# Optimization experiments

Hardware: AMD Instinct MI355X
Metric: run time of the kernel (lower is better)

## Reference

```python
import jax, jax.numpy as jnp
import numpy as np

N_E, E_DIM = 1024, 256

def setup_inputs() -> dict:
    key = jax.random.key(0)
    k1, k2 = jax.random.split(key)
    z = jax.random.normal(k1, (16, E_DIM, 64, 64), dtype=jnp.float32)
    codebook = jax.random.normal(k2, (N_E, E_DIM), dtype=jnp.float32)
    return {"z": z, "codebook": codebook}

def reference(z, codebook):
    B, C, H, W = z.shape  # C == e_dim
    zp = jnp.transpose(z, (0, 2, 3, 1))          # B,H,W,C
    zf = zp.reshape(-1, C)                        # N,C with N=B*H*W
    # L2 distance: ||z||^2 + ||c||^2 - 2 z c^T  -> [N, n_e]
    d = (jnp.sum(zf * zf, axis=1, keepdims=True)
         + jnp.sum(codebook * codebook, axis=1)
         - 2.0 * jnp.matmul(zf, codebook.T))
    idx = jnp.argmin(d, axis=1)                   # [N] int
    # one-hot @ codebook == gather (same math)
    z_q = codebook[idx].reshape(zp.shape)         # B,H,W,C
    codebook_loss = jnp.mean((z_q - jax.lax.stop_gradient(zp)) ** 2)
    z_q_out = jnp.transpose(z_q, (0, 3, 1, 2))    # B,C,H,W
    min_encoding_indices = idx.reshape(B, 1, H, W)
    return (z_q_out, codebook_loss, jnp.zeros((), z_q_out.dtype), min_encoding_indices)
```

## Files before the change

kernel.cpp:

```cpp
#include <hip/hip_runtime.h>

#define HW 4096
#define NE 1024
#define LOSS_OFF 16777216
#define IDX_OFF  16777218
#define MARGIN 0.08f

typedef __attribute__((ext_vector_type(8))) _Float16 half8v;
typedef __attribute__((ext_vector_type(4))) float float4v;

#define WS_LIST_OFF   64
#define WS_CNORM_OFF  262208
#define WS_CBH_OFF    266304
#define WS_PART_OFF   790592

__device__ __forceinline__ unsigned short f16rne(float f) {
    _Float16 h = (_Float16)f;
    return __builtin_bit_cast(unsigned short, h);
}

__device__ __forceinline__ unsigned f16pk(float a, float b) {
    auto h = __builtin_amdgcn_cvt_pkrtz(a, b);
    return __builtin_bit_cast(unsigned, h);
}

__device__ __forceinline__ void stage16(const void* g, void* l) {
    __builtin_amdgcn_global_load_lds(
        (const __attribute__((address_space(1))) unsigned*)g,
        (__attribute__((address_space(3))) unsigned*)l, 16, 0, 0);
}

__global__ __launch_bounds__(256) void k0_prep(const float* __restrict__ cb,
                                               float* __restrict__ cnorm,
                                               unsigned short* __restrict__ cbh,
                                               int* __restrict__ flagcnt) {
    const int tid = threadIdx.x;
    if (blockIdx.x == 0 && tid == 0) *flagcnt = 0;
    const int e = blockIdx.x * 64 + (tid >> 2);
    const int j = tid & 3;
    const float4* src = (const float4*)(cb + (size_t)e * 256 + j * 64);
    unsigned short* dst = cbh + (size_t)e * 256 + j * 64;
    float s = 0.f;
#pragma unroll
    for (int i = 0; i < 16; ++i) {
        float4 v = src[i];
        s += v.x * v.x + v.y * v.y + v.z * v.z + v.w * v.w;
        unsigned p0 = (unsigned)f16rne(v.x) | ((unsigned)f16rne(v.y) << 16);
        unsigned p1 = (unsigned)f16rne(v.z) | ((unsigned)f16rne(v.w) << 16);
        *(uint2*)(dst + i * 4) = make_uint2(p0, p1);
    }
    s += __shfl_xor(s, 1, 64);
    s += __shfl_xor(s, 2, 64);
    if (j == 0) cnorm[e] = 0.5f * s;
}

__global__ __launch_bounds__(256, 3) void k1_mfma(const float* __restrict__ z,
                                                  const unsigned short* __restrict__ cbh,
                                                  const float* __restrict__ cnorm,
                                                  float* __restrict__ out_idx,
                                                  int* __restrict__ flagcnt,
                                                  int* __restrict__ flaglist) {
    __shared__ __align__(16) char smem[34304];
    char* bufs = smem;
    float* cand1 = (float*)(smem + 32768);
    int*   candi = (int*)  (smem + 33280);
    float* cand2 = (float*)(smem + 33792);

    const int tid = threadIdx.x;
    const int lane = tid & 63, w = tid >> 6;
    const int wx = w & 1, wy = w >> 1;
    const int lr = lane & 15, lg = lane >> 4;
    const unsigned bswz = (unsigned)(lr << 4);

    const int n0 = blockIdx.x * 64;
    const int hw0 = n0 & 4095;
    const float* zb = z + (size_t)(n0 >> 12) * (256 * HW);
    const char* cbh_b = (const char*)cbh;

    {
        const int row = tid & 63, kg8 = tid >> 6;
        const unsigned zswz = (unsigned)((row & 15) << 4);
#pragma unroll
        for (int it = 0; it < 8; ++it) {
            int kb = (kg8 + it * 4) * 8;
            float v[8];
#pragma unroll
            for (int q = 0; q < 8; ++q) v[q] = zb[(size_t)(kb + q) * HW + hw0 + row];
            unsigned pk[4];
#pragma unroll
            for (int q = 0; q < 4; ++q) pk[q] = f16pk(v[2*q], v[2*q+1]);
            unsigned scol = (unsigned)(kb * 2) ^ zswz;
            *(int4*)(smem + row * 512 + scol) = make_int4(pk[0], pk[1], pk[2], pk[3]);
        }
    }
    __syncthreads();

    half8v A[2][8];
#pragma unroll
    for (int mi = 0; mi < 2; ++mi)
#pragma unroll
        for (int ks = 0; ks < 8; ++ks)
            A[mi][ks] = *(const half8v*)(smem + (32*wy + 16*mi + lr) * 512
                                              + ((unsigned)(64*ks + 16*lg) ^ bswz));
    __syncthreads();

    const int i0 = w * 4;
    const int elo_half = lane >> 5;
    const unsigned col0 = (unsigned)((lane & 31) * 16);

#pragma unroll
    for (int i = 0; i < 4; ++i) {
        int e_loc = 2 * (i0 + i) + elo_half;
        unsigned col = col0 ^ (unsigned)((e_loc & 15) << 4);
        stage16(cbh_b + (size_t)e_loc * 512 + col, bufs + (i0 + i) * 1024);
    }
    __syncthreads();

    const float* cnp = cnorm + 16 * wx + lr;
    float b1[8], b2[8]; int bi[8];
#pragma unroll
    for (int i = 0; i < 8; ++i) { b1[i] = 1e30f; b2[i] = 1e30f; bi[i] = 0; }

    for (int c = 0; c < 32; ++c) {
        if (c < 31) {
            char* nb = bufs + ((c + 1) & 1) * 16384;
            const size_t ebase = (size_t)(c + 1) * 32;
#pragma unroll
            for (int i = 0; i < 4; ++i) {
                int e_loc = 2 * (i0 + i) + elo_half;
                unsigned col = col0 ^ (unsigned)((e_loc & 15) << 4);
                stage16(cbh_b + (ebase + e_loc) * 512 + col, nb + (i0 + i) * 1024);
            }
        }

        const char* bp = bufs + (c & 1) * 16384 + (16 * wx + lr) * 512;
        float4v a0 = {0.f,0.f,0.f,0.f}, a1 = a0;
#pragma unroll
        for (int ks = 0; ks < 8; ++ks) {
            half8v B = *(const half8v*)(bp + ((unsigned)(64*ks + 16*lg) ^ bswz));
            a0 = __builtin_amdgcn_mfma_f32_16x16x32_f16(A[0][ks], B, a0, 0, 0, 0);
            a1 = __builtin_amdgcn_mfma_f32_16x16x32_f16(A[1][ks], B, a1, 0, 0, 0);
        }

        const float cn = cnp[c * 32];
        const int e = c * 32 + 16 * wx + lr;
#pragma unroll
        for (int r = 0; r < 4; ++r) {
            float s0 = cn - a0[r];
            b2[r] = fminf(b2[r], fmaxf(b1[r], s0));
            if (s0 < b1[r]) { b1[r] = s0; bi[r] = e; }
            float s1 = cn - a1[r];
            b2[4+r] = fminf(b2[4+r], fmaxf(b1[4+r], s1));
            if (s1 < b1[4+r]) { b1[4+r] = s1; bi[4+r] = e; }
        }

        __syncthreads();
    }

#pragma unroll
    for (int m = 1; m <= 8; m <<= 1) {
#pragma unroll
        for (int s = 0; s < 8; ++s) {
            float o1 = __shfl_xor(b1[s], m, 64);
            float o2 = __shfl_xor(b2[s], m, 64);
            int   oi = __shfl_xor(bi[s], m, 64);
            float m2 = fminf(fmaxf(b1[s], o1), fminf(b2[s], o2));
            if (o1 < b1[s] || (o1 == b1[s] && oi < bi[s])) { b1[s] = o1; bi[s] = oi; }
            b2[s] = m2;
        }
    }
    if (lr == 0) {
#pragma unroll
        for (int mi = 0; mi < 2; ++mi)
#pragma unroll
            for (int r = 0; r < 4; ++r) {
                int row = 32 * wy + 16 * mi + 4 * lg + r;
                cand1[row * 2 + wx] = b1[mi * 4 + r];
                cand2[row * 2 + wx] = b2[mi * 4 + r];
                candi[row * 2 + wx] = bi[mi * 4 + r];
            }
    }
    __syncthreads();
    if (tid < 64) {
        float s1a = cand1[tid * 2], s1b = cand1[tid * 2 + 1];
        int   ia = candi[tid * 2],  ib = candi[tid * 2 + 1];
        float s2 = fminf(fminf(cand2[tid * 2], cand2[tid * 2 + 1]), fmaxf(s1a, s1b));
        float s1; int iw;
        if (s1b < s1a || (s1b == s1a && ib < ia)) { s1 = s1b; iw = ib; }
        else { s1 = s1a; iw = ia; }
        out_idx[n0 + tid] = (float)iw;
        if (s2 - s1 < MARGIN) {
            int p = atomicAdd(flagcnt, 1);
            flaglist[p] = n0 + tid;
        }
    }
}

__global__ __launch_bounds__(256) void k1b_refine(const float* __restrict__ z,
                                                  const float* __restrict__ cb,
                                                  const float* __restrict__ cnorm,
                                                  const int* __restrict__ flagcnt,
                                                  const int* __restrict__ flaglist,
                                                  float* __restrict__ out_idx) {
    __shared__ float zr[4][260];
    __shared__ int   rows[4];
    __shared__ float wb[4][4];
    __shared__ int   wi[4][4];
    const int tid = threadIdx.x;
    const int lane = tid & 63, w = tid >> 6;
    const int gid = tid >> 2, j = tid & 3;
    const int count = *flagcnt;
    for (int base = blockIdx.x * 4; base < count; base += gridDim.x * 4) {
        const int nr = min(4, count - base);
        __syncthreads();
        if (tid < nr) rows[tid] = flaglist[base + tid];
        __syncthreads();
        for (int r = 0; r < nr; ++r) {
            const int n = rows[r];
            zr[r][tid] = z[((size_t)(n >> 12) * 256 + tid) * HW + (n & 4095)];
        }
        __syncthreads();

        float acc[16][4];
#pragma unroll
        for (int p = 0; p < 16; ++p)
#pragma unroll
            for (int r = 0; r < 4; ++r) acc[p][r] = 0.f;

        const char* cbase = (const char*)cb + (size_t)gid * 1024 + j * 16;
#pragma unroll 2
        for (int q = 0; q < 16; ++q) {
            float4 zv[4];
#pragma unroll
            for (int r = 0; r < 4; ++r) zv[r] = *(const float4*)(&zr[r][q * 16 + j * 4]);
#pragma unroll
            for (int p = 0; p < 16; ++p) {
                float4 c = *(const float4*)(cbase + (size_t)p * 65536 + q * 64);
#pragma unroll
                for (int r = 0; r < 4; ++r) {
                    float a = acc[p][r];
                    a = fmaf(zv[r].x, c.x, a);
                    a = fmaf(zv[r].y, c.y, a);
                    a = fmaf(zv[r].z, c.z, a);
                    a = fmaf(zv[r].w, c.w, a);
                    acc[p][r] = a;
                }
            }
        }

        float best[4]; int bidx[4];
#pragma unroll
        for (int r = 0; r < 4; ++r) { best[r] = 1e30f; bidx[r] = 0; }
#pragma unroll
        for (int p = 0; p < 16; ++p) {
            const int e = p * 64 + gid;
            const float cn = cnorm[e];
#pragma unroll
            for (int r = 0; r < 4; ++r) {
                float d = acc[p][r];
                d += __shfl_xor(d, 1, 64);
                d += __shfl_xor(d, 2, 64);
                float s = cn - d;
                if (s < best[r]) { best[r] = s; bidx[r] = e; }
            }
        }
#pragma unroll
        for (int m = 1; m <= 32; m <<= 1) {
#pragma unroll
            for (int r = 0; r < 4; ++r) {
                float ob = __shfl_xor(best[r], m, 64);
                int   oi = __shfl_xor(bidx[r], m, 64);
                if (ob < best[r] || (ob == best[r] && oi < bidx[r])) { best[r] = ob; bidx[r] = oi; }
            }
        }
        if (lane == 0) {
#pragma unroll
            for (int r = 0; r < 4; ++r) { wb[w][r] = best[r]; wi[w][r] = bidx[r]; }
        }
        __syncthreads();
        if (tid < nr) {
            float bb = wb[0][tid]; int ii = wi[0][tid];
#pragma unroll
            for (int q = 1; q < 4; ++q)
                if (wb[q][tid] < bb || (wb[q][tid] == bb && wi[q][tid] < ii)) { bb = wb[q][tid]; ii = wi[q][tid]; }
            out_idx[rows[tid]] = (float)ii;
        }
        __syncthreads();
    }
}

__global__ __launch_bounds__(256) void k2_scatter(const float* __restrict__ z,
                                                  const float* __restrict__ cb,
                                                  const float* __restrict__ idxf,
                                                  float* __restrict__ zq,
                                                  float* __restrict__ part) {
    __shared__ float cbrow[64][257];
    __shared__ int   earr[64];
    __shared__ float ls[4];
    const int tid = threadIdx.x;
    const int b = blockIdx.x >> 6;
    const int hw0 = (blockIdx.x & 63) * 64;

    if (tid < 64) earr[tid] = (int)idxf[b * 4096 + hw0 + tid];
    __syncthreads();
    {
        const int r = tid >> 2, qd = tid & 3;
        const float4* src = (const float4*)(cb + (size_t)earr[r] * 256 + qd * 64);
#pragma unroll
        for (int i = 0; i < 16; ++i) {
            float4 v = src[i];
            float* d = &cbrow[r][qd * 64 + i * 4];
            d[0] = v.x; d[1] = v.y; d[2] = v.z; d[3] = v.w;
        }
    }
    __syncthreads();

    const int hw = tid & 63, cq = tid >> 6;
    const size_t zbase = ((size_t)b * 256) * 4096 + hw0 + hw;
    float lsum = 0.f;
#pragma unroll 8
    for (int pass = 0; pass < 64; ++pass) {
        const int c = pass * 4 + cq;
        const size_t flat = zbase + (size_t)c * 4096;
        float q = cbrow[hw][c];
        zq[flat] = q;
        float d = q - z[flat];
        lsum = fmaf(d, d, lsum);
    }
#pragma unroll
    for (int m = 32; m >= 1; m >>= 1) lsum += __shfl_down(lsum, m, 64);
    const int lane = tid & 63, w = tid >> 6;
    if (lane == 0) ls[w] = lsum;
    __syncthreads();
    if (tid == 0) part[blockIdx.x] = ls[0] + ls[1] + ls[2] + ls[3];
}

__global__ __launch_bounds__(256) void k3_final(const float* __restrict__ part,
                                                float* __restrict__ dout) {
    __shared__ float ls[4];
    float s = 0.f;
#pragma unroll
    for (int it = 0; it < 4; ++it) s += part[threadIdx.x + it * 256];
#pragma unroll
    for (int m = 32; m >= 1; m >>= 1) s += __shfl_down(s, m, 64);
    int lane = threadIdx.x & 63, w = threadIdx.x >> 6;
    if (lane == 0) ls[w] = s;
    __syncthreads();
    if (threadIdx.x == 0) {
        float total = ls[0] + ls[1] + ls[2] + ls[3];
        dout[LOSS_OFF]     = total / 16777216.0f;
        dout[LOSS_OFF + 1] = 0.0f;
    }
}

extern "C" void kernel_launch(void* const* d_in, const int* in_sizes, int n_in,
                              void* d_out, int out_size, void* d_ws, size_t ws_size,
                              hipStream_t stream) {
    const float* z  = (const float*)d_in[0];
    const float* cb = (const float*)d_in[1];
    float* out = (float*)d_out;
    char* ws = (char*)d_ws;

    int*            flagcnt  = (int*)ws;
    int*            flaglist = (int*)(ws + WS_LIST_OFF);
    float*          cnorm    = (float*)(ws + WS_CNORM_OFF);
    unsigned short* cbh      = (unsigned short*)(ws + WS_CBH_OFF);
    float*          part     = (float*)(ws + WS_PART_OFF);

    hipLaunchKernelGGL(k0_prep,   dim3(16),   dim3(256), 0, stream, cb, cnorm, cbh, flagcnt);
    hipLaunchKernelGGL(k1_mfma,   dim3(1024), dim3(256), 0, stream,
                       z, cbh, cnorm, out + IDX_OFF, flagcnt, flaglist);
    hipLaunchKernelGGL(k1b_refine, dim3(2048), dim3(256), 0, stream,
                       z, cb, cnorm, flagcnt, flaglist, out + IDX_OFF);
    hipLaunchKernelGGL(k2_scatter, dim3(1024), dim3(256), 0, stream,
                       z, cb, out + IDX_OFF, out, part);
    hipLaunchKernelGGL(k3_final,  dim3(1),    dim3(256), 0, stream, part, out);
}
```

Baseline: 131.8 us.

## Double k1 block to 128 rows with 8 waves and fold final loss reduction into scatter

The distance/argmin kernel now processes 128 z rows per block with 512 threads (8 waves), so each staged codebook chunk in LDS is reused by twice as many rows and fewer blocks are launched. The launch bound changes from (256,3) to (512,4) and LDS use grows to 64KB. Separately, the tiny final loss kernel is removed: the last scatter block, found with an atomic counter plus threadfence, sums the partials. This saves a launch, at the cost of the fence and the atomic. The larger LDS footprint may limit how many blocks fit per CU. The codebook-staging loop now covers only 2 of the 4 chunks per wave, which matches 8 waves covering 16 rows.

```diff
diff --git a/kernel.cpp b/kernel.cpp
--- a/kernel.cpp
+++ b/kernel.cpp
@@ -9,6 +9,7 @@
 typedef __attribute__((ext_vector_type(8))) _Float16 half8v;
 typedef __attribute__((ext_vector_type(4))) float float4v;
 
+#define WS_K2CNT_OFF  16
 #define WS_LIST_OFF   64
 #define WS_CNORM_OFF  262208
 #define WS_CBH_OFF    266304
@@ -33,9 +34,10 @@
 __global__ __launch_bounds__(256) void k0_prep(const float* __restrict__ cb,
                                                float* __restrict__ cnorm,
                                                unsigned short* __restrict__ cbh,
-                                               int* __restrict__ flagcnt) {
+                                               int* __restrict__ flagcnt,
+                                               int* __restrict__ k2cnt) {
     const int tid = threadIdx.x;
-    if (blockIdx.x == 0 && tid == 0) *flagcnt = 0;
+    if (blockIdx.x == 0 && tid == 0) { *flagcnt = 0; *k2cnt = 0; }
     const int e = blockIdx.x * 64 + (tid >> 2);
     const int j = tid & 3;
     const float4* src = (const float4*)(cb + (size_t)e * 256 + j * 64);
@@ -54,35 +56,35 @@
     if (j == 0) cnorm[e] = 0.5f * s;
 }
 
-__global__ __launch_bounds__(256, 3) void k1_mfma(const float* __restrict__ z,
+__global__ __launch_bounds__(512, 4) void k1_mfma(const float* __restrict__ z,
                                                   const unsigned short* __restrict__ cbh,
                                                   const float* __restrict__ cnorm,
                                                   float* __restrict__ out_idx,
                                                   int* __restrict__ flagcnt,
                                                   int* __restrict__ flaglist) {
-    __shared__ __align__(16) char smem[34304];
+    __shared__ __align__(16) char smem[65536];
     char* bufs = smem;
-    float* cand1 = (float*)(smem + 32768);
-    int*   candi = (int*)  (smem + 33280);
-    float* cand2 = (float*)(smem + 33792);
+    float* cand1 = (float*)(smem + 49152);
+    int*   candi = (int*)  (smem + 50176);
+    float* cand2 = (float*)(smem + 51200);
 
     const int tid = threadIdx.x;
-    const int lane = tid & 63, w = tid >> 6;
-    const int wx = w & 1, wy = w >> 1;
+    const int lane = tid & 63, wid = tid >> 6;
+    const int wx = wid & 1, wy = wid >> 1;
     const int lr = lane & 15, lg = lane >> 4;
     const unsigned bswz = (unsigned)(lr << 4);
 
-    const int n0 = blockIdx.x * 64;
+    const int n0 = blockIdx.x * 128;
     const int hw0 = n0 & 4095;
     const float* zb = z + (size_t)(n0 >> 12) * (256 * HW);
     const char* cbh_b = (const char*)cbh;
 
     {
-        const int row = tid & 63, kg8 = tid >> 6;
+        const int row = tid & 127, kgrp = tid >> 7;
         const unsigned zswz = (unsigned)((row & 15) << 4);
 #pragma unroll
         for (int it = 0; it < 8; ++it) {
-            int kb = (kg8 + it * 4) * 8;
+            int kb = (kgrp + it * 4) * 8;
             float v[8];
 #pragma unroll
             for (int q = 0; q < 8; ++q) v[q] = zb[(size_t)(kb + q) * HW + hw0 + row];
@@ -104,15 +106,15 @@
                                               + ((unsigned)(64*ks + 16*lg) ^ bswz));
     __syncthreads();
 
-    const int i0 = w * 4;
     const int elo_half = lane >> 5;
     const unsigned col0 = (unsigned)((lane & 31) * 16);
 
 #pragma unroll
-    for (int i = 0; i < 4; ++i) {
-        int e_loc = 2 * (i0 + i) + elo_half;
+    for (int ii = 0; ii < 2; ++ii) {
+        int i = 2 * wid + ii;
+        int e_loc = 2 * i + elo_half;
         unsigned col = col0 ^ (unsigned)((e_loc & 15) << 4);
-        stage16(cbh_b + (size_t)e_loc * 512 + col, bufs + (i0 + i) * 1024);
+        stage16(cbh_b + (size_t)e_loc * 512 + col, bufs + i * 1024);
     }
     __syncthreads();
 
@@ -126,10 +128,11 @@
             char* nb = bufs + ((c + 1) & 1) * 16384;
             const size_t ebase = (size_t)(c + 1) * 32;
 #pragma unroll
-            for (int i = 0; i < 4; ++i) {
-                int e_loc = 2 * (i0 + i) + elo_half;
+            for (int ii = 0; ii < 2; ++ii) {
+                int i = 2 * wid + ii;
+                int e_loc = 2 * i + elo_half;
                 unsigned col = col0 ^ (unsigned)((e_loc & 15) << 4);
-                stage16(cbh_b + (ebase + e_loc) * 512 + col, nb + (i0 + i) * 1024);
+                stage16(cbh_b + (ebase + e_loc) * 512 + col, nb + i * 1024);
             }
         }
 
@@ -181,7 +184,7 @@
             }
     }
     __syncthreads();
-    if (tid < 64) {
+    if (tid < 128) {
         float s1a = cand1[tid * 2], s1b = cand1[tid * 2 + 1];
         int   ia = candi[tid * 2],  ib = candi[tid * 2 + 1];
         float s2 = fminf(fminf(cand2[tid * 2], cand2[tid * 2 + 1]), fmaxf(s1a, s1b));
@@ -293,10 +296,13 @@
                                                   const float* __restrict__ cb,
                                                   const float* __restrict__ idxf,
                                                   float* __restrict__ zq,
-                                                  float* __restrict__ part) {
+                                                  float* __restrict__ part,
+                                                  int* __restrict__ k2cnt,
+                                                  float* __restrict__ dout) {
     __shared__ float cbrow[64][257];
     __shared__ int   earr[64];
     __shared__ float ls[4];
+    __shared__ int   lastBlk;
     const int tid = threadIdx.x;
     const int b = blockIdx.x >> 6;
     const int hw0 = (blockIdx.x & 63) * 64;
@@ -332,24 +338,24 @@
     const int lane = tid & 63, w = tid >> 6;
     if (lane == 0) ls[w] = lsum;
     __syncthreads();
-    if (tid == 0) part[blockIdx.x] = ls[0] + ls[1] + ls[2] + ls[3];
-}
-
-__global__ __launch_bounds__(256) void k3_final(const float* __restrict__ part,
-                                                float* __restrict__ dout) {
-    __shared__ float ls[4];
-    float s = 0.f;
-#pragma unroll
-    for (int it = 0; it < 4; ++it) s += part[threadIdx.x + it * 256];
-#pragma unroll
-    for (int m = 32; m >= 1; m >>= 1) s += __shfl_down(s, m, 64);
-    int lane = threadIdx.x & 63, w = threadIdx.x >> 6;
-    if (lane == 0) ls[w] = s;
-    __syncthreads();
-    if (threadIdx.x == 0) {
-        float total = ls[0] + ls[1] + ls[2] + ls[3];
-        dout[LOSS_OFF]     = total / 16777216.0f;
-        dout[LOSS_OFF + 1] = 0.0f;
+    if (tid == 0) {
+        part[blockIdx.x] = ls[0] + ls[1] + ls[2] + ls[3];
+        __threadfence();
+        int old = atomicAdd(k2cnt, 1);
+        lastBlk = (old == (int)gridDim.x - 1);
+    }
+    __syncthreads();
+    if (lastBlk) {
+        float s = part[tid] + part[tid + 256] + part[tid + 512] + part[tid + 768];
+#pragma unroll
+        for (int m = 32; m >= 1; m >>= 1) s += __shfl_down(s, m, 64);
+        if (lane == 0) ls[w] = s;
+        __syncthreads();
+        if (tid == 0) {
+            float total = ls[0] + ls[1] + ls[2] + ls[3];
+            dout[LOSS_OFF]     = total / 16777216.0f;
+            dout[LOSS_OFF + 1] = 0.0f;
+        }
     }
 }
 
@@ -362,17 +368,17 @@
     char* ws = (char*)d_ws;
 
     int*            flagcnt  = (int*)ws;
+    int*            k2cnt    = (int*)(ws + WS_K2CNT_OFF);
     int*            flaglist = (int*)(ws + WS_LIST_OFF);
     float*          cnorm    = (float*)(ws + WS_CNORM_OFF);
     unsigned short* cbh      = (unsigned short*)(ws + WS_CBH_OFF);
     float*          part     = (float*)(ws + WS_PART_OFF);
 
-    hipLaunchKernelGGL(k0_prep,   dim3(16),   dim3(256), 0, stream, cb, cnorm, cbh, flagcnt);
-    hipLaunchKernelGGL(k1_mfma,   dim3(1024), dim3(256), 0, stream,
+    hipLaunchKernelGGL(k0_prep,   dim3(16),   dim3(256), 0, stream, cb, cnorm, cbh, flagcnt, k2cnt);
+    hipLaunchKernelGGL(k1_mfma,   dim3(512),  dim3(512), 0, stream,
                        z, cbh, cnorm, out + IDX_OFF, flagcnt, flaglist);
     hipLaunchKernelGGL(k1b_refine, dim3(2048), dim3(256), 0, stream,
                        z, cb, cnorm, flagcnt, flaglist, out + IDX_OFF);
     hipLaunchKernelGGL(k2_scatter, dim3(1024), dim3(256), 0, stream,
-                       z, cb, out + IDX_OFF, out, part);
-    hipLaunchKernelGGL(k3_final,  dim3(1),    dim3(256), 0, stream, part, out);
-}
+                       z, cb, out + IDX_OFF, out, part, k2cnt, out);
+}
```

Result: slower. 158.9 us (+20.6%).
